# Kernel optimization log

Measured on AMD Instinct MI355X. Metric: run time of the kernel, lower is better.

The kernel has to match this reference:

```python
import jax, jax.numpy as jnp
import numpy as np

EPS = 1e-7  # Keras K.epsilon()
ROUTINGS = 3

def squash(v, axis=-1):
    s2 = jnp.sum(jnp.square(v), axis=axis, keepdims=True)
    scale = s2 / (1.0 + s2) / jnp.sqrt(s2 + EPS)
    return scale * v

def setup_inputs() -> dict:
    key = jax.random.key(0)
    k1, k2 = jax.random.split(key)
    inputs = jax.random.normal(k1, (64, 1152, 8), dtype=jnp.float32)
    W = jax.random.normal(k2, (8, 43, 16), dtype=jnp.float32) * 0.1  # glorot-ish scale
    return {"inputs": inputs, "W": W}

def reference(inputs, W):
    # inputs: [b, i, j] (batch, input_num_capsule, input_dim_capsule)
    # W: [j, k, l] -> inputs_hat: [b, i, k, l]
    inputs_hat = jnp.einsum('bij,jkl->bikl', inputs, W)
    b_sz, I, N, _ = inputs_hat.shape
    b = jnp.zeros((b_sz, I, N), dtype=inputs_hat.dtype)
    outputs = None
    for r in range(ROUTINGS):
        c = jax.nn.softmax(b, axis=2)                       # [b, i, k]
        s = jnp.einsum('bik,bikl->bkl', c, inputs_hat)      # [b, k, l]
        outputs = squash(s, axis=-1)                         # [b, k, l]
        if r < ROUTINGS - 1:
            agreement = jnp.einsum('bikl,bkl->bik', inputs_hat, outputs)
            b = b + agreement
    return outputs
```

## Files before the change

### kernel.cpp

```cpp
#include <hip/hip_runtime.h>

#define EPS 1e-7f
#define NB 64
#define NI 1152
#define NJ 8
#define NK 43
#define NL 16
#define NSLICE 4
#define SLICE 288
#define THREADS 384
#define NKG 11
#define CPS 292
#define GPS 33
#define PARTS 344
#define WVSZ 352

__device__ __forceinline__ void routing_main(
    int tid, const float4* __restrict__ sXa, const float4* __restrict__ sXb,
    const float (* __restrict__ sWv)[44], float4* __restrict__ cP,
    float* __restrict__ gpOut)
{
    float a[44];
    if (tid < SLICE) {
        float4 x0 = sXa[tid], x1 = sXb[tid];
        float xr[NJ] = {x0.x, x0.y, x0.z, x0.w, x1.x, x1.y, x1.z, x1.w};
        #pragma unroll
        for (int k = 0; k < 44; ++k) a[k] = 0.f;
        #pragma unroll
        for (int j = 0; j < NJ; ++j) {
            #pragma unroll
            for (int k4 = 0; k4 < NKG; ++k4) {
                float4 wv = *(const float4*)&sWv[j][k4*4];
                a[k4*4+0] = fmaf(xr[j], wv.x, a[k4*4+0]);
                a[k4*4+1] = fmaf(xr[j], wv.y, a[k4*4+1]);
                a[k4*4+2] = fmaf(xr[j], wv.z, a[k4*4+2]);
                a[k4*4+3] = fmaf(xr[j], wv.w, a[k4*4+3]);
            }
        }
        float m0=a[0], m1=a[1], m2=a[2], m3=a[3];
        #pragma unroll
        for (int k = 4; k < 40; k += 4) {
            m0 = fmaxf(m0, a[k+0]); m1 = fmaxf(m1, a[k+1]);
            m2 = fmaxf(m2, a[k+2]); m3 = fmaxf(m3, a[k+3]);
        }
        m0 = fmaxf(m0, a[40]); m1 = fmaxf(m1, a[41]); m2 = fmaxf(m2, a[42]);
        const float m = fmaxf(fmaxf(m0, m1), fmaxf(m2, m3));
        float z0=0.f, z1=0.f, z2=0.f, z3=0.f;
        #pragma unroll
        for (int k = 0; k < 40; k += 4) {
            a[k+0] = __expf(a[k+0]-m); z0 += a[k+0];
            a[k+1] = __expf(a[k+1]-m); z1 += a[k+1];
            a[k+2] = __expf(a[k+2]-m); z2 += a[k+2];
            a[k+3] = __expf(a[k+3]-m); z3 += a[k+3];
        }
        a[40] = __expf(a[40]-m); z0 += a[40];
        a[41] = __expf(a[41]-m); z1 += a[41];
        a[42] = __expf(a[42]-m); z2 += a[42];
        const float inv = 1.f / ((z0+z1) + (z2+z3));
        #pragma unroll
        for (int k = 0; k < NK; ++k) a[k] *= inv;
        a[43] = 0.f;
        #pragma unroll
        for (int kg = 0; kg < NKG; ++kg)
            cP[kg*CPS + tid] = make_float4(a[4*kg], a[4*kg+1], a[4*kg+2], a[4*kg+3]);
    }
    __syncthreads();
    float acc[4][8];
    #pragma unroll
    for (int q = 0; q < 4; ++q)
        #pragma unroll
        for (int j = 0; j < 8; ++j) acc[q][j] = 0.f;
    if (tid < 352) {
        const int kg = tid >> 5, s = tid & 31;
        #pragma unroll
        for (int ii = 0; ii < SLICE/32; ++ii) {
            const int il = s + 32*ii;
            float4 c4 = cP[kg*CPS + il];
            float4 xa = sXa[il], xb = sXb[il];
            acc[0][0]=fmaf(c4.x,xa.x,acc[0][0]); acc[0][1]=fmaf(c4.x,xa.y,acc[0][1]);
            acc[0][2]=fmaf(c4.x,xa.z,acc[0][2]); acc[0][3]=fmaf(c4.x,xa.w,acc[0][3]);
            acc[0][4]=fmaf(c4.x,xb.x,acc[0][4]); acc[0][5]=fmaf(c4.x,xb.y,acc[0][5]);
            acc[0][6]=fmaf(c4.x,xb.z,acc[0][6]); acc[0][7]=fmaf(c4.x,xb.w,acc[0][7]);
            acc[1][0]=fmaf(c4.y,xa.x,acc[1][0]); acc[1][1]=fmaf(c4.y,xa.y,acc[1][1]);
            acc[1][2]=fmaf(c4.y,xa.z,acc[1][2]); acc[1][3]=fmaf(c4.y,xa.w,acc[1][3]);
            acc[1][4]=fmaf(c4.y,xb.x,acc[1][4]); acc[1][5]=fmaf(c4.y,xb.y,acc[1][5]);
            acc[1][6]=fmaf(c4.y,xb.z,acc[1][6]); acc[1][7]=fmaf(c4.y,xb.w,acc[1][7]);
            acc[2][0]=fmaf(c4.z,xa.x,acc[2][0]); acc[2][1]=fmaf(c4.z,xa.y,acc[2][1]);
            acc[2][2]=fmaf(c4.z,xa.z,acc[2][2]); acc[2][3]=fmaf(c4.z,xa.w,acc[2][3]);
            acc[2][4]=fmaf(c4.z,xb.x,acc[2][4]); acc[2][5]=fmaf(c4.z,xb.y,acc[2][5]);
            acc[2][6]=fmaf(c4.z,xb.z,acc[2][6]); acc[2][7]=fmaf(c4.z,xb.w,acc[2][7]);
            acc[3][0]=fmaf(c4.w,xa.x,acc[3][0]); acc[3][1]=fmaf(c4.w,xa.y,acc[3][1]);
            acc[3][2]=fmaf(c4.w,xa.z,acc[3][2]); acc[3][3]=fmaf(c4.w,xa.w,acc[3][3]);
            acc[3][4]=fmaf(c4.w,xb.x,acc[3][4]); acc[3][5]=fmaf(c4.w,xb.y,acc[3][5]);
            acc[3][6]=fmaf(c4.w,xb.z,acc[3][6]); acc[3][7]=fmaf(c4.w,xb.w,acc[3][7]);
        }
    }
    __syncthreads();
    float* Gp = (float*)cP;
    if (tid < 352) {
        #pragma unroll
        for (int q = 0; q < 4; ++q)
            #pragma unroll
            for (int j = 0; j < 8; ++j)
                Gp[tid*GPS + q*8 + j] = acc[q][j];
    }
    __syncthreads();
    if (tid < PARTS) {
        const int k = tid >> 3, j = tid & 7;
        const int kg = k >> 2, k4 = k & 3;
        float g = 0.f;
        #pragma unroll 8
        for (int s = 0; s < 32; ++s) g += Gp[(kg*32 + s)*GPS + k4*8 + j];
        gpOut[tid] = g;
    }
}

__device__ __forceinline__ void load_slice(int tid, const float* Xb, int sl,
                                           float4* sXa, float4* sXb) {
    const float4* Xs4 = (const float4*)(Xb + (size_t)sl*SLICE*NJ);
    for (int t = tid; t < SLICE*2; t += THREADS) {
        float4 v = Xs4[t];
        if (t & 1) sXb[t >> 1] = v; else sXa[t >> 1] = v;
    }
}

__device__ __forceinline__ void squash_block(int tid, const float (*sS)[NL], float (*sV)[NL]) {
    if (tid < NK) {
        float s2 = 0.f;
        #pragma unroll
        for (int l = 0; l < NL; ++l) { float v = sS[tid][l]; s2 += v*v; }
        float scale = s2 / ((1.f + s2) * sqrtf(s2 + EPS));
        #pragma unroll
        for (int l = 0; l < NL; ++l) sV[tid][l] = scale * sS[tid][l];
    }
}

__global__ __launch_bounds__(THREADS, 1)
void caps_k1(const float* __restrict__ X, const float* __restrict__ W,
             float* __restrict__ wv0, float* __restrict__ gp1) {
    __shared__ __align__(16) float4 sXa[SLICE], sXb[SLICE];
    __shared__ __align__(16) float4 cP[NKG*CPS];
    __shared__ __align__(16) float sWv[NJ][44];
    __shared__ __align__(16) float sS[NK][NL];
    __shared__ __align__(16) float sV[NK][NL];
    __shared__ float sXs[NJ];

    const int tid = threadIdx.x;
    const int b  = blockIdx.x >> 2;
    const int sl = blockIdx.x & 3;
    const float* Xb = X + (size_t)b * (NI*NJ);

    load_slice(tid, Xb, sl, sXa, sXb);
    {
        float* red = (float*)cP;
        const int j = tid / 48, sub = tid % 48;
        float p = 0.f;
        #pragma unroll
        for (int ii = 0; ii < NI/48; ++ii) p += Xb[(sub + 48*ii)*NJ + j];
        red[j*48 + sub] = p;
    }
    __syncthreads();
    if (tid < NJ) {
        const float* red = (const float*)cP;
        float s = 0.f;
        for (int q = 0; q < 48; ++q) s += red[tid*48 + q];
        sXs[tid] = s;
    }
    __syncthreads();
    for (int t = tid; t < NK*NL; t += THREADS) {
        float s = 0.f;
        #pragma unroll
        for (int j = 0; j < NJ; ++j) s += sXs[j] * W[j*NK*NL + t];
        sS[t >> 4][t & 15] = s * (1.0f/43.0f);
    }
    __syncthreads();
    squash_block(tid, sS, sV);
    __syncthreads();
    if (tid < WVSZ) {
        const int j = tid / 44, k = tid % 44;
        float wv = 0.f;
        if (k < NK) {
            const float4* Wr = (const float4*)(W + j*NK*NL + k*NL);
            #pragma unroll
            for (int l4 = 0; l4 < 4; ++l4) {
                float4 w = Wr[l4];
                const float4 vv = *(const float4*)&sV[k][l4*4];
                wv += w.x*vv.x + w.y*vv.y + w.z*vv.z + w.w*vv.w;
            }
        }
        sWv[j][k] = wv;
        if (sl == 0) wv0[(size_t)b*WVSZ + tid] = wv;
    }
    __syncthreads();
    routing_main(tid, sXa, sXb, sWv, cP, gp1 + (size_t)(b*NSLICE + sl)*PARTS);
}

__global__ __launch_bounds__(THREADS, 1)
void caps_k2(const float* __restrict__ X, const float* __restrict__ W,
             const float* __restrict__ wv0, const float* __restrict__ gp1,
             float* __restrict__ gp2) {
    __shared__ __align__(16) float4 sXa[SLICE], sXb[SLICE];
    __shared__ __align__(16) float4 cP[NKG*CPS];
    __shared__ __align__(16) float sWv[NJ][44];
    __shared__ __align__(16) float sS[NK][NL];
    __shared__ __align__(16) float sV[NK][NL];
    __shared__ float sG[PARTS];

    const int tid = threadIdx.x;
    const int b  = blockIdx.x >> 2;
    const int sl = blockIdx.x & 3;
    const float* Xb = X + (size_t)b * (NI*NJ);

    load_slice(tid, Xb, sl, sXa, sXb);
    if (tid < PARTS) {
        float g = 0.f;
        #pragma unroll
        for (int q = 0; q < NSLICE; ++q) g += gp1[(size_t)(b*NSLICE + q)*PARTS + tid];
        sG[tid] = g;
    }
    __syncthreads();
    for (int t = tid; t < NK*NL; t += THREADS) {
        const int k = t >> 4;
        float s = 0.f;
        #pragma unroll
        for (int j = 0; j < NJ; ++j) s = fmaf(sG[k*8+j], W[j*NK*NL + t], s);
        sS[k][t & 15] = s;
    }
    __syncthreads();
    squash_block(tid, sS, sV);
    __syncthreads();
    if (tid < WVSZ) {
        const int j = tid / 44, k = tid % 44;
        float wv = 0.f;
        if (k < NK) {
            const float4* Wr = (const float4*)(W + j*NK*NL + k*NL);
            #pragma unroll
            for (int l4 = 0; l4 < 4; ++l4) {
                float4 w = Wr[l4];
                const float4 vv = *(const float4*)&sV[k][l4*4];
                wv += w.x*vv.x + w.y*vv.y + w.z*vv.z + w.w*vv.w;
            }
        }
        sWv[j][k] = wv0[(size_t)b*WVSZ + tid] + wv;
    }
    __syncthreads();
    routing_main(tid, sXa, sXb, sWv, cP, gp2 + (size_t)(b*NSLICE + sl)*PARTS);
}

__global__ __launch_bounds__(THREADS, 1)
void caps_k3(const float* __restrict__ W, const float* __restrict__ gp2,
             float* __restrict__ out) {
    __shared__ float sG[PARTS];
    __shared__ __align__(16) float sS[NK][NL];
    __shared__ __align__(16) float sV[NK][NL];
    const int tid = threadIdx.x;
    const int b = blockIdx.x;
    if (tid < PARTS) {
        float g = 0.f;
        #pragma unroll
        for (int q = 0; q < NSLICE; ++q) g += gp2[(size_t)(b*NSLICE + q)*PARTS + tid];
        sG[tid] = g;
    }
    __syncthreads();
    for (int t = tid; t < NK*NL; t += THREADS) {
        const int k = t >> 4;
        float s = 0.f;
        #pragma unroll
        for (int j = 0; j < NJ; ++j) s = fmaf(sG[k*8+j], W[j*NK*NL + t], s);
        sS[k][t & 15] = s;
    }
    __syncthreads();
    squash_block(tid, sS, sV);
    __syncthreads();
    for (int t = tid; t < NK*NL; t += THREADS)
        out[(size_t)b*NK*NL + t] = sV[t >> 4][t & 15];
}

extern "C" void kernel_launch(void* const* d_in, const int* in_sizes, int n_in,
                              void* d_out, int out_size, void* d_ws, size_t ws_size,
                              hipStream_t stream) {
    const float* X = (const float*)d_in[0];
    const float* W = (const float*)d_in[1];
    float* out = (float*)d_out;
    float* wv0 = (float*)d_ws;
    float* gp1 = wv0 + NB*WVSZ;
    float* gp2 = gp1 + NB*NSLICE*PARTS;
    hipLaunchKernelGGL(caps_k1, dim3(NB*NSLICE), dim3(THREADS), 0, stream, X, W, wv0, gp1);
    hipLaunchKernelGGL(caps_k2, dim3(NB*NSLICE), dim3(THREADS), 0, stream, X, W, wv0, gp1, gp2);
    hipLaunchKernelGGL(caps_k3, dim3(NB), dim3(THREADS), 0, stream, W, gp2, out);
}
```

Baseline: 26.76 us.

## Split batches into eight slices and replace shared-memory reductions with wave shuffles

Doubles the number of input-capsule slices per batch so the grid has twice as many smaller blocks, and raises launch bounds to allow three blocks per CU. The partial-sum reduction in routing now uses a register transpose-reduce with shuffles instead of staging through shared memory with extra barriers. Squash is fused into the s computation via 16-lane shuffle reductions, and the initial column sum of X uses vector loads plus shuffles. The cost is more partial buffers to sum across slices, and fewer active threads per block in the routing phase.

```diff
diff --git a/kernel.cpp b/kernel.cpp
--- a/kernel.cpp
+++ b/kernel.cpp
@@ -6,24 +6,43 @@
 #define NJ 8
 #define NK 43
 #define NL 16
-#define NSLICE 4
-#define SLICE 288
+#define KL (NK*NL)
+#define NSLICE 8
+#define SLICE 144
 #define THREADS 384
 #define NKG 11
-#define CPS 292
-#define GPS 33
+#define CPS 148
 #define PARTS 344
 #define WVSZ 352
+#define SVP 17
+
+__device__ __forceinline__ void load_slice(int tid, const float* __restrict__ Xb, int sl,
+                                           float4* sXa, float4* sXb) {
+    if (tid < SLICE*2) {
+        const float4* Xs4 = (const float4*)(Xb + (size_t)sl*SLICE*NJ);
+        float4 v = Xs4[tid];
+        if (tid & 1) sXb[tid >> 1] = v; else sXa[tid >> 1] = v;
+    }
+}
+
+__device__ __forceinline__ float squash_scale(float sv) {
+    float sq = sv * sv;
+    sq += __shfl_xor(sq, 1);
+    sq += __shfl_xor(sq, 2);
+    sq += __shfl_xor(sq, 4);
+    sq += __shfl_xor(sq, 8);
+    const float scale = sq / ((1.f + sq) * sqrtf(sq + EPS));
+    return scale * sv;
+}
 
 __device__ __forceinline__ void routing_main(
-    int tid, const float4* __restrict__ sXa, const float4* __restrict__ sXb,
-    const float (* __restrict__ sWv)[44], float4* __restrict__ cP,
-    float* __restrict__ gpOut)
+    int tid, const float4* sXa, const float4* sXb,
+    const float (*sWv)[44], float4* cP, float* __restrict__ gpOut)
 {
-    float a[44];
     if (tid < SLICE) {
         float4 x0 = sXa[tid], x1 = sXb[tid];
         float xr[NJ] = {x0.x, x0.y, x0.z, x0.w, x1.x, x1.y, x1.z, x1.w};
+        float a[44];
         #pragma unroll
         for (int k = 0; k < 44; ++k) a[k] = 0.f;
         #pragma unroll
@@ -65,16 +84,16 @@
             cP[kg*CPS + tid] = make_float4(a[4*kg], a[4*kg+1], a[4*kg+2], a[4*kg+3]);
     }
     __syncthreads();
-    float acc[4][8];
-    #pragma unroll
-    for (int q = 0; q < 4; ++q)
-        #pragma unroll
-        for (int j = 0; j < 8; ++j) acc[q][j] = 0.f;
-    if (tid < 352) {
-        const int kg = tid >> 5, s = tid & 31;
-        #pragma unroll
-        for (int ii = 0; ii < SLICE/32; ++ii) {
-            const int il = s + 32*ii;
+    if (tid < NKG*16) {
+        const int kg = tid >> 4, s = tid & 15;
+        float acc[4][8];
+        #pragma unroll
+        for (int q = 0; q < 4; ++q)
+            #pragma unroll
+            for (int j = 0; j < 8; ++j) acc[q][j] = 0.f;
+        #pragma unroll
+        for (int ii = 0; ii < SLICE/16; ++ii) {
+            const int il = s + 16*ii;
             float4 c4 = cP[kg*CPS + il];
             float4 xa = sXa[il], xb = sXb[il];
             acc[0][0]=fmaf(c4.x,xa.x,acc[0][0]); acc[0][1]=fmaf(c4.x,xa.y,acc[0][1]);
@@ -94,121 +113,123 @@
             acc[3][4]=fmaf(c4.w,xb.x,acc[3][4]); acc[3][5]=fmaf(c4.w,xb.y,acc[3][5]);
             acc[3][6]=fmaf(c4.w,xb.z,acc[3][6]); acc[3][7]=fmaf(c4.w,xb.w,acc[3][7]);
         }
-    }
-    __syncthreads();
-    float* Gp = (float*)cP;
-    if (tid < 352) {
+        float cur[32];
         #pragma unroll
         for (int q = 0; q < 4; ++q)
             #pragma unroll
-            for (int j = 0; j < 8; ++j)
-                Gp[tid*GPS + q*8 + j] = acc[q][j];
-    }
-    __syncthreads();
-    if (tid < PARTS) {
-        const int k = tid >> 3, j = tid & 7;
-        const int kg = k >> 2, k4 = k & 3;
-        float g = 0.f;
-        #pragma unroll 8
-        for (int s = 0; s < 32; ++s) g += Gp[(kg*32 + s)*GPS + k4*8 + j];
-        gpOut[tid] = g;
-    }
-}
-
-__device__ __forceinline__ void load_slice(int tid, const float* Xb, int sl,
-                                           float4* sXa, float4* sXb) {
-    const float4* Xs4 = (const float4*)(Xb + (size_t)sl*SLICE*NJ);
-    for (int t = tid; t < SLICE*2; t += THREADS) {
-        float4 v = Xs4[t];
-        if (t & 1) sXb[t >> 1] = v; else sXa[t >> 1] = v;
-    }
-}
-
-__device__ __forceinline__ void squash_block(int tid, const float (*sS)[NL], float (*sV)[NL]) {
-    if (tid < NK) {
-        float s2 = 0.f;
-        #pragma unroll
-        for (int l = 0; l < NL; ++l) { float v = sS[tid][l]; s2 += v*v; }
-        float scale = s2 / ((1.f + s2) * sqrtf(s2 + EPS));
-        #pragma unroll
-        for (int l = 0; l < NL; ++l) sV[tid][l] = scale * sS[tid][l];
-    }
-}
-
-__global__ __launch_bounds__(THREADS, 1)
+            for (int j = 0; j < 8; ++j) cur[q*8+j] = acc[q][j];
+        {   const bool up = (tid & 8) != 0;
+            #pragma unroll
+            for (int v = 0; v < 16; ++v) {
+                float give = up ? cur[v] : cur[v+16];
+                float keep = up ? cur[v+16] : cur[v];
+                cur[v] = keep + __shfl_xor(give, 8);
+            } }
+        {   const bool up = (tid & 4) != 0;
+            #pragma unroll
+            for (int v = 0; v < 8; ++v) {
+                float give = up ? cur[v] : cur[v+8];
+                float keep = up ? cur[v+8] : cur[v];
+                cur[v] = keep + __shfl_xor(give, 4);
+            } }
+        {   const bool up = (tid & 2) != 0;
+            #pragma unroll
+            for (int v = 0; v < 4; ++v) {
+                float give = up ? cur[v] : cur[v+4];
+                float keep = up ? cur[v+4] : cur[v];
+                cur[v] = keep + __shfl_xor(give, 2);
+            } }
+        {   const bool up = (tid & 1) != 0;
+            #pragma unroll
+            for (int v = 0; v < 2; ++v) {
+                float give = up ? cur[v] : cur[v+2];
+                float keep = up ? cur[v+2] : cur[v];
+                cur[v] = keep + __shfl_xor(give, 1);
+            } }
+        const int p = kg*32 + (s << 1);
+        if (p < PARTS)
+            *(float2*)&gpOut[p] = make_float2(cur[0], cur[1]);
+    }
+}
+
+__global__ __launch_bounds__(THREADS, 3)
 void caps_k1(const float* __restrict__ X, const float* __restrict__ W,
-             float* __restrict__ wv0, float* __restrict__ gp1) {
+             float* __restrict__ wv0g, float* __restrict__ gp1) {
     __shared__ __align__(16) float4 sXa[SLICE], sXb[SLICE];
     __shared__ __align__(16) float4 cP[NKG*CPS];
     __shared__ __align__(16) float sWv[NJ][44];
-    __shared__ __align__(16) float sS[NK][NL];
-    __shared__ __align__(16) float sV[NK][NL];
+    __shared__ __align__(16) float sV[NK*SVP];
+    __shared__ __align__(16) float4 xsW[12];
     __shared__ float sXs[NJ];
 
     const int tid = threadIdx.x;
-    const int b  = blockIdx.x >> 2;
-    const int sl = blockIdx.x & 3;
+    const int b  = blockIdx.x >> 3;
+    const int sl = blockIdx.x & 7;
     const float* Xb = X + (size_t)b * (NI*NJ);
 
     load_slice(tid, Xb, sl, sXa, sXb);
     {
-        float* red = (float*)cP;
-        const int j = tid / 48, sub = tid % 48;
-        float p = 0.f;
-        #pragma unroll
-        for (int ii = 0; ii < NI/48; ++ii) p += Xb[(sub + 48*ii)*NJ + j];
-        red[j*48 + sub] = p;
+        const float4* X4 = (const float4*)Xb;
+        float4 ax = X4[tid];
+        #pragma unroll
+        for (int r = 1; r < 6; ++r) {
+            float4 v = X4[tid + r*THREADS];
+            ax.x += v.x; ax.y += v.y; ax.z += v.z; ax.w += v.w;
+        }
+        #pragma unroll
+        for (int msk = 2; msk <= 32; msk <<= 1) {
+            ax.x += __shfl_xor(ax.x, msk);
+            ax.y += __shfl_xor(ax.y, msk);
+            ax.z += __shfl_xor(ax.z, msk);
+            ax.w += __shfl_xor(ax.w, msk);
+        }
+        if ((tid & 63) < 2) xsW[(tid >> 6)*2 + (tid & 1)] = ax;
     }
     __syncthreads();
     if (tid < NJ) {
-        const float* red = (const float*)cP;
+        const float* f = (const float*)xsW;
         float s = 0.f;
-        for (int q = 0; q < 48; ++q) s += red[tid*48 + q];
+        #pragma unroll
+        for (int w = 0; w < 6; ++w) s += f[(w*2 + (tid >> 2))*4 + (tid & 3)];
         sXs[tid] = s;
     }
     __syncthreads();
-    for (int t = tid; t < NK*NL; t += THREADS) {
-        float s = 0.f;
-        #pragma unroll
-        for (int j = 0; j < NJ; ++j) s += sXs[j] * W[j*NK*NL + t];
-        sS[t >> 4][t & 15] = s * (1.0f/43.0f);
-    }
-    __syncthreads();
-    squash_block(tid, sS, sV);
+    for (int t = tid; t < KL; t += THREADS) {
+        float sv = 0.f;
+        #pragma unroll
+        for (int j = 0; j < NJ; ++j) sv = fmaf(sXs[j], W[j*KL + t], sv);
+        sv *= (1.0f/43.0f);
+        sV[(t >> 4)*SVP + (t & 15)] = squash_scale(sv);
+    }
     __syncthreads();
     if (tid < WVSZ) {
         const int j = tid / 44, k = tid % 44;
         float wv = 0.f;
         if (k < NK) {
-            const float4* Wr = (const float4*)(W + j*NK*NL + k*NL);
-            #pragma unroll
-            for (int l4 = 0; l4 < 4; ++l4) {
-                float4 w = Wr[l4];
-                const float4 vv = *(const float4*)&sV[k][l4*4];
-                wv += w.x*vv.x + w.y*vv.y + w.z*vv.z + w.w*vv.w;
-            }
-        }
-        sWv[j][k] = wv;
-        if (sl == 0) wv0[(size_t)b*WVSZ + tid] = wv;
+            #pragma unroll
+            for (int l = 0; l < NL; ++l)
+                wv = fmaf(W[j*KL + k*NL + l], sV[k*SVP + l], wv);
+        }
+        ((float*)sWv)[tid] = wv;
+        if (sl == 0) wv0g[(size_t)b*WVSZ + tid] = wv;
     }
     __syncthreads();
     routing_main(tid, sXa, sXb, sWv, cP, gp1 + (size_t)(b*NSLICE + sl)*PARTS);
 }
 
-__global__ __launch_bounds__(THREADS, 1)
+__global__ __launch_bounds__(THREADS, 3)
 void caps_k2(const float* __restrict__ X, const float* __restrict__ W,
-             const float* __restrict__ wv0, const float* __restrict__ gp1,
+             const float* __restrict__ wv0g, const float* __restrict__ gp1,
              float* __restrict__ gp2) {
     __shared__ __align__(16) float4 sXa[SLICE], sXb[SLICE];
     __shared__ __align__(16) float4 cP[NKG*CPS];
     __shared__ __align__(16) float sWv[NJ][44];
-    __shared__ __align__(16) float sS[NK][NL];
-    __shared__ __align__(16) float sV[NK][NL];
+    __shared__ __align__(16) float sV[NK*SVP];
     __shared__ float sG[PARTS];
 
     const int tid = threadIdx.x;
-    const int b  = blockIdx.x >> 2;
-    const int sl = blockIdx.x & 3;
+    const int b  = blockIdx.x >> 3;
+    const int sl = blockIdx.x & 7;
     const float* Xb = X + (size_t)b * (NI*NJ);
 
     load_slice(tid, Xb, sl, sXa, sXb);
@@ -219,29 +240,23 @@
         sG[tid] = g;
     }
     __syncthreads();
-    for (int t = tid; t < NK*NL; t += THREADS) {
-        const int k = t >> 4;
-        float s = 0.f;
-        #pragma unroll
-        for (int j = 0; j < NJ; ++j) s = fmaf(sG[k*8+j], W[j*NK*NL + t], s);
-        sS[k][t & 15] = s;
-    }
-    __syncthreads();
-    squash_block(tid, sS, sV);
+    for (int t = tid; t < KL; t += THREADS) {
+        const int k8 = (t >> 4)*8;
+        float sv = 0.f;
+        #pragma unroll
+        for (int j = 0; j < NJ; ++j) sv = fmaf(sG[k8 + j], W[j*KL + t], sv);
+        sV[(t >> 4)*SVP + (t & 15)] = squash_scale(sv);
+    }
     __syncthreads();
     if (tid < WVSZ) {
         const int j = tid / 44, k = tid % 44;
         float wv = 0.f;
         if (k < NK) {
-            const float4* Wr = (const float4*)(W + j*NK*NL + k*NL);
-            #pragma unroll
-            for (int l4 = 0; l4 < 4; ++l4) {
-                float4 w = Wr[l4];
-                const float4 vv = *(const float4*)&sV[k][l4*4];
-                wv += w.x*vv.x + w.y*vv.y + w.z*vv.z + w.w*vv.w;
-            }
-        }
-        sWv[j][k] = wv0[(size_t)b*WVSZ + tid] + wv;
+            #pragma unroll
+            for (int l = 0; l < NL; ++l)
+                wv = fmaf(W[j*KL + k*NL + l], sV[k*SVP + l], wv);
+        }
+        ((float*)sWv)[tid] = wv0g[(size_t)b*WVSZ + tid] + wv;
     }
     __syncthreads();
     routing_main(tid, sXa, sXb, sWv, cP, gp2 + (size_t)(b*NSLICE + sl)*PARTS);
@@ -251,8 +266,6 @@
 void caps_k3(const float* __restrict__ W, const float* __restrict__ gp2,
              float* __restrict__ out) {
     __shared__ float sG[PARTS];
-    __shared__ __align__(16) float sS[NK][NL];
-    __shared__ __align__(16) float sV[NK][NL];
     const int tid = threadIdx.x;
     const int b = blockIdx.x;
     if (tid < PARTS) {
@@ -262,18 +275,13 @@
         sG[tid] = g;
     }
     __syncthreads();
-    for (int t = tid; t < NK*NL; t += THREADS) {
-        const int k = t >> 4;
-        float s = 0.f;
-        #pragma unroll
-        for (int j = 0; j < NJ; ++j) s = fmaf(sG[k*8+j], W[j*NK*NL + t], s);
-        sS[k][t & 15] = s;
-    }
-    __syncthreads();
-    squash_block(tid, sS, sV);
-    __syncthreads();
-    for (int t = tid; t < NK*NL; t += THREADS)
-        out[(size_t)b*NK*NL + t] = sV[t >> 4][t & 15];
+    for (int t = tid; t < KL; t += THREADS) {
+        const int k8 = (t >> 4)*8;
+        float sv = 0.f;
+        #pragma unroll
+        for (int j = 0; j < NJ; ++j) sv = fmaf(sG[k8 + j], W[j*KL + t], sv);
+        out[(size_t)b*KL + t] = squash_scale(sv);
+    }
 }
 
 extern "C" void kernel_launch(void* const* d_in, const int* in_sizes, int n_in,
```

Measured after the change: 24.97 us, median of 2. 6.7% less time.
